# Optimization experiments

Measured on AMD Instinct MI355X. Metric: run time of the kernel, lower is better.

Reference implementation:

```python
import jax, jax.numpy as jnp
import numpy as np

MIN_NORM = 1e-15
EPS = 1e-7          # fp32 eps used by hgcn Hyperboloid
MAX_NORM = 1e6
C = 1.0             # curvature for all layers (args.c = 1)
N, D = 16384, 64

# ---- Hyperboloid manifold ops (faithful to hgcn manifolds/hyperboloid.py) ----

def _norm(v):
    return jnp.sqrt(jnp.sum(v * v, axis=-1, keepdims=True))

def proj(x, c):
    K = 1.0 / c
    y = x[..., 1:]
    x0 = jnp.sqrt(jnp.clip(K + jnp.sum(y * y, -1, keepdims=True), EPS))
    return jnp.concatenate([x0, y], -1)

def proj_tan0(u, c):
    return jnp.concatenate([jnp.zeros_like(u[..., :1]), u[..., 1:]], -1)

def expmap0(u, c):
    sqrtK = (1.0 / c) ** 0.5
    x = u[..., 1:]
    xn = jnp.clip(_norm(x), MIN_NORM)
    theta = xn / sqrtK
    res = jnp.concatenate([sqrtK * jnp.cosh(theta),
                           sqrtK * jnp.sinh(theta) * x / xn], -1)
    return proj(res, c)

def logmap0(x, c):
    sqrtK = (1.0 / c) ** 0.5
    y = x[..., 1:]
    yn = jnp.clip(_norm(y), MIN_NORM)
    theta = jnp.clip(x[..., :1] / sqrtK, 1.0 + EPS)
    return jnp.concatenate([jnp.zeros_like(theta),
                            sqrtK * jnp.arccosh(theta) * y / yn], -1)

def mink_dot(x, y):
    return -x[..., :1] * y[..., :1] + jnp.sum(x[..., 1:] * y[..., 1:], -1, keepdims=True)

def expmap(u, x, c):
    sqrtK = (1.0 / c) ** 0.5
    normu = jnp.minimum(jnp.sqrt(jnp.clip(mink_dot(u, u), EPS)), MAX_NORM)
    theta = jnp.clip(normu / sqrtK, MIN_NORM)
    return proj(jnp.cosh(theta) * x + jnp.sinh(theta) * u / theta, c)

def proj_tan(u, x, c):
    ux = jnp.sum(x[..., 1:] * u[..., 1:], -1, keepdims=True)
    return jnp.concatenate([ux / jnp.clip(x[..., :1], EPS), u[..., 1:]], -1)

def ptransp0(x, u, c):
    sqrtK = (1.0 / c) ** 0.5
    x0, y = x[..., :1], x[..., 1:]
    yn = jnp.clip(_norm(y), MIN_NORM)
    yhat = y / yn
    v = jnp.concatenate([-yn, (sqrtK - x0) * yhat], -1)
    alpha = jnp.sum(yhat * u[..., 1:], -1, keepdims=True) / sqrtK
    return proj_tan(u - alpha * v, x, c)

def mobius_add(x, y, c):
    u = logmap0(y, c)
    v = ptransp0(x, u, c)
    return expmap(v, x, c)

# ---- HGCN layers (HypLinear -> HypAgg -> HypAct), dropout=0, use_att=False ----

def hyp_linear(x, W, b, c):
    mv = expmap0(logmap0(x, c) @ W.T, c)   # mobius_matvec
    res = proj(mv, c)
    hyp_bias = proj(expmap0(proj_tan0(b[None, :], c), c), c)
    return proj(mobius_add(res, hyp_bias, c), c)

def hyp_agg(x, adj_n, c):
    return proj(expmap0(adj_n @ logmap0(x, c), c), c)

def hyp_act(x, c_in, c_out):
    xt = proj_tan0(jax.nn.relu(logmap0(x, c_in)), c_out)
    return proj(expmap0(xt, c_out), c_out)

def hgc_layer(x, adj_n, W, b, c_in, c_out):
    h = hyp_linear(x, W, b, c_in)
    h = hyp_agg(h, adj_n, c_in)
    return hyp_act(h, c_in, c_out)

def setup_inputs() -> dict:
    key = jax.random.key(0)
    k1, k2, k3, k4, k5, k6 = jax.random.split(key, 6)
    return {
        "x": jax.random.normal(k1, (N, D), jnp.float32),
        "adj": jax.random.uniform(k2, (N, N), jnp.float32),
        "W1": jax.random.normal(k3, (D, D), jnp.float32) * 0.125,
        "b1": jax.random.normal(k4, (D,), jnp.float32) * 0.01,
        "W2": jax.random.normal(k5, (D, D), jnp.float32) * 0.125,
        "b2": jax.random.normal(k6, (D,), jnp.float32) * 0.01,
    }

def reference(x, adj, W1, b1, W2, b2):
    # project input to hyperboloid
    x_hyp = proj(expmap0(proj_tan0(x, C), C), C)
    # row-normalize adjacency: D^{-1} A (inf -> 0)
    rsum = jnp.sum(adj, axis=1)
    rinv = jnp.where(rsum != 0, 1.0 / rsum, 0.0)
    adj_n = rinv[:, None] * adj
    h1 = hgc_layer(x_hyp, adj_n, W1, b1, C, C)
    h2 = hgc_layer(h1, adj_n, W2, b2, C, C)
    return (h1, h2)
```

## Files before the change

kernel.cpp:

```cpp
#include <hip/hip_runtime.h>
#include <cstdint>
#include <cstddef>

#define NROWS 16384
#define KDIM  16384
#define EPSF  1e-7f
#define MINN  1e-15f
#define MAXN  1e6f
#define BM    32
#define BK2   64
#define NSTEP2 (KDIM/BK2)
#define APG   528
#define BPG   1040
#define ABUF  (8*APG)
#define BBUF  (8*BPG)

typedef __attribute__((ext_vector_type(8))) short short8;
typedef __attribute__((ext_vector_type(4))) float f32x4;
typedef __attribute__((ext_vector_type(4))) unsigned short u16x4;

__device__ __forceinline__ unsigned short f2bf(float f){
  union { float f; unsigned u; } c; c.f = f;
  unsigned u = c.u;
  unsigned r = (u + 0x7FFFu + ((u >> 16) & 1u)) >> 16;
  return (unsigned short)r;
}

__device__ __forceinline__ float wredsum(float v){
  v += __shfl_xor(v, 1);
  v += __shfl_xor(v, 2);
  v += __shfl_xor(v, 4);
  v += __shfl_xor(v, 8);
  v += __shfl_xor(v, 16);
  v += __shfl_xor(v, 32);
  return v;
}

__global__ __launch_bounds__(128) void k_bias(const float* __restrict__ b1,
                                              const float* __restrict__ b2,
                                              float* __restrict__ ub){
  int w = threadIdx.x >> 6, l = threadIdx.x & 63;
  const float* b = w ? b2 : b1;
  float bv = b[l];
  float tb = l ? bv : 0.f;
  float s  = wredsum(tb*tb);
  float xn = fmaxf(sqrtf(s), MINN);
  float sc = sinhf(xn)/xn;
  float e  = sc*tb;
  float s2 = wredsum(e*e);
  float x0 = sqrtf(fmaxf(1.f+s2, EPSF));
  float yn = fmaxf(sqrtf(s2), MINN);
  float th = fmaxf(x0, 1.f+EPSF);
  float u  = l ? acoshf(th)*e/yn : 0.f;
  ub[w*64 + l] = u;
}

template<int MODE>
__global__ __launch_bounds__(256) void k_linear(const float* __restrict__ in,
                                                const float* __restrict__ W,
                                                const float* __restrict__ ub,
                                                float* __restrict__ g){
  __shared__ float Wt[64*65];
  int tid = threadIdx.x;
  for(int idx = tid; idx < 4096; idx += 256){
    int j = idx >> 6, k = idx & 63;
    Wt[k*65 + j] = W[idx];
  }
  __syncthreads();
  int lane = tid & 63;
  int row  = blockIdx.x*4 + (tid >> 6);
  float v = in[(size_t)row*64 + lane];
  float lx;
  if (MODE == 0){
    float t  = lane ? v : 0.f;
    float s  = wredsum(t*t);
    float tn = fmaxf(sqrtf(s), MINN);
    float sc = sinhf(tn)/tn;
    float e  = sc*t;
    float s2 = wredsum(e*e);
    float x0 = sqrtf(fmaxf(1.f+s2, EPSF));
    float yn = fmaxf(sqrtf(s2), MINN);
    float th = fmaxf(x0, 1.f+EPSF);
    lx = lane ? acoshf(th)*e/yn : 0.f;
  } else {
    float t  = lane ? v : 0.f;
    float s2 = wredsum(t*t);
    float x0 = __shfl(v, 0);
    float yn = fmaxf(sqrtf(s2), MINN);
    float th = fmaxf(x0, 1.f+EPSF);
    lx = lane ? acoshf(th)*t/yn : 0.f;
  }
  float mv = 0.f;
  #pragma unroll
  for(int k = 0; k < 64; k++){
    mv = fmaf(__shfl(lx, k), Wt[k*65 + lane], mv);
  }
  float u  = lane ? mv : 0.f;
  float s  = wredsum(u*u);
  float un = fmaxf(sqrtf(s), MINN);
  float sc = sinhf(un)/un;
  float e  = sc*u;
  float s2 = wredsum(e*e);
  float r0 = sqrtf(fmaxf(1.f+s2, EPSF));
  float ubt   = lane ? ub[lane] : 0.f;
  float yn    = fmaxf(sqrtf(s2), MINN);
  float yhat  = e/yn;
  float alpha = wredsum(yhat*ubt);
  float w     = ubt - alpha*(1.f - r0)*yhat;
  float ux    = wredsum(e*w);
  float v0    = ux / fmaxf(r0, EPSF);
  float md    = wredsum(w*w) - v0*v0;
  float normu = fminf(sqrtf(fmaxf(md, EPSF)), MAXN);
  float th2   = fmaxf(normu, MINN);
  float ch    = coshf(th2);
  float shq   = sinhf(th2)/th2;
  float ov    = ch*(lane ? e : r0) + shq*(lane ? w : v0);
  float ot    = lane ? ov : 0.f;
  float s3    = wredsum(ot*ot);
  float o0    = sqrtf(fmaxf(1.f+s3, EPSF));
  float yn2 = fmaxf(sqrtf(s3), MINN);
  float th3 = fmaxf(o0, 1.f+EPSF);
  float gv  = lane ? acoshf(th3)*ot/yn2 : 0.f;
  g[(size_t)row*64 + lane] = gv;
}

__global__ __launch_bounds__(256) void k_tr(const float* __restrict__ g,
                                            short* __restrict__ gT){
  __shared__ float t[64][65];
  int tid = threadIdx.x;
  int b   = blockIdx.x;
  int r   = tid >> 2;
  int c0  = (tid & 3)*16;
  const float* src = g + ((size_t)b*64 + r)*64 + c0;
  #pragma unroll
  for(int i = 0; i < 4; i++){
    float4 v = *(const float4*)(src + i*4);
    t[r][c0 + i*4 + 0] = v.x; t[r][c0 + i*4 + 1] = v.y;
    t[r][c0 + i*4 + 2] = v.z; t[r][c0 + i*4 + 3] = v.w;
  }
  __syncthreads();
  int n   = tid >> 2;
  int seg = tid & 3;
  short8 p0, p1;
  #pragma unroll
  for(int j = 0; j < 8; j++) p0[j] = (short)f2bf(t[seg*16 + j][n]);
  #pragma unroll
  for(int j = 0; j < 8; j++) p1[j] = (short)f2bf(t[seg*16 + 8 + j][n]);
  short* dst = gT + (size_t)n*KDIM + b*64 + seg*16;
  *(short8*)(dst)     = p0;
  *(short8*)(dst + 8) = p1;
}

template<bool FIRST>
__global__ __launch_bounds__(512) void k_matmul(const float* __restrict__ adj,
                                                const short* __restrict__ gT,
                                                float* __restrict__ agg,
                                                float* __restrict__ prsum){
  __shared__ __align__(16) char lds[2*ABUF + 2*BBUF];
  char* Abase = lds;
  char* Bbase = lds + 2*ABUF;
  int tid  = threadIdx.x;
  int lane = tid & 63, w = tid >> 6;
  int row0 = blockIdx.x * BM;

  int r  = tid >> 4;
  int kq = tid & 15;
  const float* ap = adj + (size_t)(row0 + r)*KDIM + kq*4;
  int AwOff = (kq >> 1)*APG + r*16 + (kq & 1)*8;

  int nB = tid & 63;
  int q2 = tid >> 6;
  const short* bp = gT + (size_t)nB*KDIM + q2*8;
  int BwOff = q2*BPG + nB*16;

  int wm = w >> 2, wn = w & 3;
  int fr = lane & 15, fk = lane >> 4;
  int ArdOff = fk*APG + (wm*16 + fr)*16;
  int BrdOff = fk*BPG + (wn*16 + fr)*16;

  f32x4 acc = {0.f,0.f,0.f,0.f};
  float rs = 0.f;

  float4 a0 = *(const float4*)(ap);
  short8 b0 = *(const short8*)(bp);
  if (FIRST) rs += a0.x + a0.y + a0.z + a0.w;
  u16x4 ak0 = { f2bf(a0.x), f2bf(a0.y), f2bf(a0.z), f2bf(a0.w) };
  *(u16x4*)(Abase + AwOff) = ak0;
  *(short8*)(Bbase + BwOff) = b0;
  float4 aR = *(const float4*)(ap + BK2);
  short8 bR = *(const short8*)(bp + BK2);
  if (FIRST) rs += aR.x + aR.y + aR.z + aR.w;
  __syncthreads();

  for (int i = 0; i < NSTEP2; i++){
    const char* Ab = Abase + (i & 1)*ABUF;
    const char* Bb = Bbase + (i & 1)*BBUF;
    short8 af0 = *(const short8*)(Ab + ArdOff);
    short8 af1 = *(const short8*)(Ab + ArdOff + 4*APG);
    short8 bf0 = *(const short8*)(Bb + BrdOff);
    short8 bf1 = *(const short8*)(Bb + BrdOff + 4*BPG);
    float4 aN; short8 bN;
    if (i + 2 < NSTEP2){
      aN = *(const float4*)(ap + (size_t)(i+2)*BK2);
      bN = *(const short8*)(bp + (size_t)(i+2)*BK2);
      if (FIRST) rs += aN.x + aN.y + aN.z + aN.w;
    }
    acc = __builtin_amdgcn_mfma_f32_16x16x32_bf16(af0, bf0, acc, 0, 0, 0);
    acc = __builtin_amdgcn_mfma_f32_16x16x32_bf16(af1, bf1, acc, 0, 0, 0);
    if (i + 1 < NSTEP2){
      char* Aw = Abase + ((i+1) & 1)*ABUF;
      char* Bw = Bbase + ((i+1) & 1)*BBUF;
      u16x4 ak = { f2bf(aR.x), f2bf(aR.y), f2bf(aR.z), f2bf(aR.w) };
      *(u16x4*)(Aw + AwOff) = ak;
      *(short8*)(Bw + BwOff) = bR;
      aR = aN; bR = bN;
    }
    __syncthreads();
  }

  if (FIRST){
    rs += __shfl_xor(rs, 1);
    rs += __shfl_xor(rs, 2);
    rs += __shfl_xor(rs, 4);
    rs += __shfl_xor(rs, 8);
    if ((lane & 15) == 0) prsum[row0 + r] = rs;
  }
  float* ob = agg + (size_t)(row0 + wm*16)*64 + wn*16;
  #pragma unroll
  for(int q = 0; q < 4; q++){
    ob[(size_t)((lane >> 4)*4 + q)*64 + (lane & 15)] = acc[q];
  }
}

template<int LAYER>
__global__ __launch_bounds__(256) void k_post(const float* __restrict__ agg,
                                              const float* __restrict__ prsum,
                                              float* __restrict__ rinv,
                                              float* __restrict__ h){
  int tid = threadIdx.x; int lane = tid & 63;
  int row = blockIdx.x*4 + (tid >> 6);
  float s = agg[(size_t)row*64 + lane];
  float ri;
  if (LAYER == 1){
    float rsum = prsum[row];
    ri = (rsum != 0.f) ? 1.f/rsum : 0.f;
    if (lane == 0) rinv[row] = ri;
  } else {
    ri = rinv[row];
  }
  float a  = s * ri;
  float at = lane ? a : 0.f;
  float ss = wredsum(at*at);
  float un = fmaxf(sqrtf(ss), MINN);
  float sc = sinhf(un)/un;
  float e  = sc*at;
  float s2 = wredsum(e*e);
  float x0 = sqrtf(fmaxf(1.f+s2, EPSF));
  float yn = fmaxf(sqrtf(s2), MINN);
  float th = fmaxf(x0, 1.f+EPSF);
  float lt = lane ? acoshf(th)*e/yn : 0.f;
  float rl = fmaxf(lt, 0.f);
  float s3 = wredsum(rl*rl);
  float rn = fmaxf(sqrtf(s3), MINN);
  float sc2= sinhf(rn)/rn;
  float e2 = sc2*rl;
  float s4 = wredsum(e2*e2);
  float h0 = sqrtf(fmaxf(1.f+s4, EPSF));
  h[(size_t)row*64 + lane] = lane ? e2 : h0;
}

extern "C" void kernel_launch(void* const* d_in, const int* in_sizes, int n_in,
                              void* d_out, int out_size, void* d_ws, size_t ws_size,
                              hipStream_t stream){
  const float* x   = (const float*)d_in[0];
  const float* adj = (const float*)d_in[1];
  const float* W1  = (const float*)d_in[2];
  const float* b1  = (const float*)d_in[3];
  const float* W2  = (const float*)d_in[4];
  const float* b2  = (const float*)d_in[5];
  float* out = (float*)d_out;
  float* h1  = out;
  float* h2  = out + (size_t)NROWS*64;

  float* wsf   = (float*)d_ws;
  float* gbuf  = wsf;
  float* aggb  = gbuf  + (size_t)NROWS*64;
  float* prsum = aggb  + (size_t)NROWS*64;
  float* rinv  = prsum + NROWS;
  float* ubs   = rinv  + NROWS;
  short* gT    = (short*)(ubs + 128);

  k_bias<<<1, 128, 0, stream>>>(b1, b2, ubs);
  k_linear<0><<<NROWS/4, 256, 0, stream>>>(x, W1, ubs, gbuf);
  k_tr<<<NROWS/64, 256, 0, stream>>>(gbuf, gT);
  k_matmul<true><<<NROWS/BM, 512, 0, stream>>>(adj, gT, aggb, prsum);
  k_post<1><<<NROWS/4, 256, 0, stream>>>(aggb, prsum, rinv, h1);
  k_linear<1><<<NROWS/4, 256, 0, stream>>>(h1, W2, ubs + 64, gbuf);
  k_tr<<<NROWS/64, 256, 0, stream>>>(gbuf, gT);
  k_matmul<false><<<NROWS/BM, 512, 0, stream>>>(adj, gT, aggb, prsum);
  k_post<2><<<NROWS/4, 256, 0, stream>>>(aggb, prsum, rinv, h2);
}
```

Measured before the change: 606.4 us.

## Cache bf16 adjacency in first matmul and reuse it in second layer

```diff
diff --git a/kernel.cpp b/kernel.cpp
--- a/kernel.cpp
+++ b/kernel.cpp
@@ -12,8 +12,12 @@
 #define NSTEP2 (KDIM/BK2)
 #define APG   528
 #define BPG   1040
-#define ABUF  (8*APG)
-#define BBUF  (8*BPG)
+#define AB1   (8*APG)
+#define BB1   (8*BPG)
+#define BKB   128
+#define NSTEPB (KDIM/BKB)
+#define AB2   (16*APG)
+#define BB2   (16*BPG)
 
 typedef __attribute__((ext_vector_type(8))) short short8;
 typedef __attribute__((ext_vector_type(4))) float f32x4;
@@ -151,14 +155,12 @@
   *(short8*)(dst + 8) = p1;
 }
 
-template<bool FIRST>
-__global__ __launch_bounds__(512) void k_matmul(const float* __restrict__ adj,
-                                                const short* __restrict__ gT,
-                                                float* __restrict__ agg,
-                                                float* __restrict__ prsum){
-  __shared__ __align__(16) char lds[2*ABUF + 2*BBUF];
-  char* Abase = lds;
-  char* Bbase = lds + 2*ABUF;
+__global__ __launch_bounds__(512) void k_matmul1(const float* __restrict__ adj,
+                                                 const short* __restrict__ gT,
+                                                 float* __restrict__ agg,
+                                                 float* __restrict__ prsum,
+                                                 short* __restrict__ adjBF){
+  __shared__ __align__(16) char lds[2*(AB1 + BB1)];
   int tid  = threadIdx.x;
   int lane = tid & 63, w = tid >> 6;
   int row0 = blockIdx.x * BM;
@@ -166,6 +168,7 @@
   int r  = tid >> 4;
   int kq = tid & 15;
   const float* ap = adj + (size_t)(row0 + r)*KDIM + kq*4;
+  short* abf = adjBF + (size_t)(row0 + r)*KDIM + kq*4;
   int AwOff = (kq >> 1)*APG + r*16 + (kq & 1)*8;
 
   int nB = tid & 63;
@@ -183,18 +186,19 @@
 
   float4 a0 = *(const float4*)(ap);
   short8 b0 = *(const short8*)(bp);
-  if (FIRST) rs += a0.x + a0.y + a0.z + a0.w;
+  rs += a0.x + a0.y + a0.z + a0.w;
   u16x4 ak0 = { f2bf(a0.x), f2bf(a0.y), f2bf(a0.z), f2bf(a0.w) };
-  *(u16x4*)(Abase + AwOff) = ak0;
-  *(short8*)(Bbase + BwOff) = b0;
+  *(u16x4*)(lds + AwOff) = ak0;
+  *(short8*)(lds + 2*AB1 + BwOff - 2*AB1 + 2*AB1) = b0;
+  *(u16x4*)(abf) = ak0;
   float4 aR = *(const float4*)(ap + BK2);
   short8 bR = *(const short8*)(bp + BK2);
-  if (FIRST) rs += aR.x + aR.y + aR.z + aR.w;
+  rs += aR.x + aR.y + aR.z + aR.w;
   __syncthreads();
 
   for (int i = 0; i < NSTEP2; i++){
-    const char* Ab = Abase + (i & 1)*ABUF;
-    const char* Bb = Bbase + (i & 1)*BBUF;
+    const char* Ab = lds + (i & 1)*AB1;
+    const char* Bb = lds + 2*AB1 + (i & 1)*BB1;
     short8 af0 = *(const short8*)(Ab + ArdOff);
     short8 af1 = *(const short8*)(Ab + ArdOff + 4*APG);
     short8 bf0 = *(const short8*)(Bb + BrdOff);
@@ -203,28 +207,102 @@
     if (i + 2 < NSTEP2){
       aN = *(const float4*)(ap + (size_t)(i+2)*BK2);
       bN = *(const short8*)(bp + (size_t)(i+2)*BK2);
-      if (FIRST) rs += aN.x + aN.y + aN.z + aN.w;
+      rs += aN.x + aN.y + aN.z + aN.w;
     }
     acc = __builtin_amdgcn_mfma_f32_16x16x32_bf16(af0, bf0, acc, 0, 0, 0);
     acc = __builtin_amdgcn_mfma_f32_16x16x32_bf16(af1, bf1, acc, 0, 0, 0);
     if (i + 1 < NSTEP2){
-      char* Aw = Abase + ((i+1) & 1)*ABUF;
-      char* Bw = Bbase + ((i+1) & 1)*BBUF;
+      char* Aw = lds + ((i+1) & 1)*AB1;
+      char* Bw = lds + 2*AB1 + ((i+1) & 1)*BB1;
       u16x4 ak = { f2bf(aR.x), f2bf(aR.y), f2bf(aR.z), f2bf(aR.w) };
       *(u16x4*)(Aw + AwOff) = ak;
       *(short8*)(Bw + BwOff) = bR;
+      *(u16x4*)(abf + (size_t)(i+1)*BK2) = ak;
       aR = aN; bR = bN;
     }
     __syncthreads();
   }
 
-  if (FIRST){
-    rs += __shfl_xor(rs, 1);
-    rs += __shfl_xor(rs, 2);
-    rs += __shfl_xor(rs, 4);
-    rs += __shfl_xor(rs, 8);
-    if ((lane & 15) == 0) prsum[row0 + r] = rs;
-  }
+  rs += __shfl_xor(rs, 1);
+  rs += __shfl_xor(rs, 2);
+  rs += __shfl_xor(rs, 4);
+  rs += __shfl_xor(rs, 8);
+  if ((lane & 15) == 0) prsum[row0 + r] = rs;
+
+  float* ob = agg + (size_t)(row0 + wm*16)*64 + wn*16;
+  #pragma unroll
+  for(int q = 0; q < 4; q++){
+    ob[(size_t)((lane >> 4)*4 + q)*64 + (lane & 15)] = acc[q];
+  }
+}
+
+__global__ __launch_bounds__(512) void k_matmul2(const short* __restrict__ adjBF,
+                                                 const short* __restrict__ gT,
+                                                 float* __restrict__ agg){
+  __shared__ __align__(16) char lds[2*(AB2 + BB2)];
+  int tid  = threadIdx.x;
+  int lane = tid & 63, w = tid >> 6;
+  int row0 = blockIdx.x * BM;
+
+  int r   = tid >> 4;
+  int s16 = tid & 15;
+  const short* ap = adjBF + (size_t)(row0 + r)*KDIM + s16*8;
+  int AwOff = s16*APG + r*16;
+
+  int nB = tid & 63;
+  int q2 = tid >> 6;
+  const short* bp = gT + (size_t)nB*KDIM + q2*8;
+  int BwOffA = q2*BPG + nB*16;
+  int BwOffB = (q2+8)*BPG + nB*16;
+
+  int wm = w >> 2, wn = w & 3;
+  int fr = lane & 15, fk = lane >> 4;
+  int ArdOff = (wm*16 + fr)*16;
+  int BrdOff = (wn*16 + fr)*16;
+
+  f32x4 acc = {0.f,0.f,0.f,0.f};
+
+  short8 aR = *(const short8*)(ap);
+  short8 bR0 = *(const short8*)(bp);
+  short8 bR1 = *(const short8*)(bp + 64);
+  *(short8*)(lds + AwOff) = aR;
+  *(short8*)(lds + 2*AB2 + BwOffA) = bR0;
+  *(short8*)(lds + 2*AB2 + BwOffB) = bR1;
+  aR  = *(const short8*)(ap + BKB);
+  bR0 = *(const short8*)(bp + BKB);
+  bR1 = *(const short8*)(bp + BKB + 64);
+  __syncthreads();
+
+  for (int i = 0; i < NSTEPB; i++){
+    const char* Ab = lds + (i & 1)*AB2;
+    const char* Bb = lds + 2*AB2 + (i & 1)*BB2;
+    short8 af[4], bf[4];
+    #pragma unroll
+    for(int kb = 0; kb < 4; kb++){
+      af[kb] = *(const short8*)(Ab + (kb*4 + fk)*APG + ArdOff);
+      bf[kb] = *(const short8*)(Bb + (kb*4 + fk)*BPG + BrdOff);
+    }
+    short8 aN, bN0, bN1;
+    if (i + 2 < NSTEPB){
+      aN  = *(const short8*)(ap + (size_t)(i+2)*BKB);
+      bN0 = *(const short8*)(bp + (size_t)(i+2)*BKB);
+      bN1 = *(const short8*)(bp + (size_t)(i+2)*BKB + 64);
+    }
+    if (i + 1 < NSTEPB){
+      char* Aw = lds + ((i+1) & 1)*AB2;
+      char* Bw = lds + 2*AB2 + ((i+1) & 1)*BB2;
+      *(short8*)(Aw + AwOff) = aR;
+      *(short8*)(Bw + BwOffA) = bR0;
+      *(short8*)(Bw + BwOffB) = bR1;
+    }
+    #pragma unroll
+    for(int kb = 0; kb < 4; kb++){
+      acc = __builtin_amdgcn_mfma_f32_16x16x32_bf16(af[kb], bf[kb], acc, 0, 0, 0);
+    }
+    aR = aN; bR0 = bN0; bR1 = bN1;
+    __syncthreads();
+  }
+
   float* ob = agg + (size_t)(row0 + wm*16)*64 + wn*16;
   #pragma unroll
   for(int q = 0; q < 4; q++){
@@ -289,14 +367,15 @@
   float* rinv  = prsum + NROWS;
   float* ubs   = rinv  + NROWS;
   short* gT    = (short*)(ubs + 128);
+  short* adjBF = gT + (size_t)64*KDIM;
 
   k_bias<<<1, 128, 0, stream>>>(b1, b2, ubs);
   k_linear<0><<<NROWS/4, 256, 0, stream>>>(x, W1, ubs, gbuf);
   k_tr<<<NROWS/64, 256, 0, stream>>>(gbuf, gT);
-  k_matmul<true><<<NROWS/BM, 512, 0, stream>>>(adj, gT, aggb, prsum);
+  k_matmul1<<<NROWS/BM, 512, 0, stream>>>(adj, gT, aggb, prsum, adjBF);
   k_post<1><<<NROWS/4, 256, 0, stream>>>(aggb, prsum, rinv, h1);
   k_linear<1><<<NROWS/4, 256, 0, stream>>>(h1, W2, ubs + 64, gbuf);
   k_tr<<<NROWS/64, 256, 0, stream>>>(gbuf, gT);
-  k_matmul<false><<<NROWS/BM, 512, 0, stream>>>(adj, gT, aggb, prsum);
+  k_matmul2<<<NROWS/BM, 512, 0, stream>>>(adjBF, gT, aggb);
   k_post<2><<<NROWS/4, 256, 0, stream>>>(aggb, prsum, rinv, h2);
 }
```

Measured after the change: 794.2 us. 31.0% more time.
